# Optimization experiments

Measured on AMD Instinct MI355X. Metric: run time of the kernel, lower is better.

Reference implementation:

```python
import jax, jax.numpy as jnp
import numpy as np

HALF = 6.0
MAXC = 63.0
M_EMA = 0.999

def _pooled_ema(feature, pre, fea):
    # feature: [b,c,64,64]; pre: [b,21,2] float coords; fea: [21,c] EMA state
    b, c, H, W = feature.shape
    x = pre[..., 0]
    y = pre[..., 1]
    # torch: clamp then .int() (truncation == floor for non-negative values)
    down = jnp.maximum(y - HALF, 0.0).astype(jnp.int32)   # [b,21]
    left = jnp.maximum(x - HALF, 0.0).astype(jnp.int32)
    upper = jnp.minimum(y + HALF, MAXC).astype(jnp.int32)
    right = jnp.minimum(x + HALF, MAXC).astype(jnp.int32)
    # divisor uses inclusive window size (s1*s2), even though the torch slice
    # feature[:, left:right, down:upper] is exclusive at right/upper (faithful quirk)
    s = ((upper - down + 1) * (right - left + 1)).astype(feature.dtype)  # [b,21]
    # integral image (padded) -> rectangle sum over [left,right) x [down,upper)
    P = jnp.pad(jnp.cumsum(jnp.cumsum(feature, axis=2), axis=3),
                ((0, 0), (0, 0), (1, 0), (1, 0)))  # [b,c,H+1,W+1]
    bi = jnp.arange(b)[:, None]  # [b,1] broadcasts with [b,21] indices
    rect = (P[bi, :, right, upper] - P[bi, :, left, upper]
            - P[bi, :, right, down] + P[bi, :, left, down])  # [b,21,c]
    f4 = rect / s[..., None]          # per-landmark average pool [b,21,c]
    fea_c = f4.mean(axis=0)           # average over batch -> [21,c]
    return M_EMA * fea_c + (1.0 - M_EMA) * fea


def setup_inputs() -> dict:
    key = jax.random.key(0)
    k1, k2, k3, k4 = jax.random.split(key, 4)
    b, c, H, W, L = 64, 256, 64, 64, 21
    f1 = jax.random.uniform(k1, (b, c, H, W), dtype=jnp.float32)
    f2 = jax.random.uniform(k2, (b, c, H, W), dtype=jnp.float32)
    pre1 = jax.random.uniform(k3, (b, L, 2), dtype=jnp.float32) * 63.0
    pre2 = jax.random.uniform(k4, (b, L, 2), dtype=jnp.float32) * 63.0
    fea1 = jnp.zeros((L, c), dtype=jnp.float32)
    fea2 = jnp.zeros((L, c), dtype=jnp.float32)
    return {"f1": f1, "f2": f2, "pre1": pre1, "pre2": pre2,
            "fea1": fea1, "fea2": fea2}


def reference(f1, f2, pre1, pre2, fea1, fea2):
    fea_c1 = _pooled_ema(f1, pre1, fea1)               # [21,c]
    log_p = jax.nn.log_softmax(fea_c1, axis=-1)
    fea_c2 = _pooled_ema(f2, pre2, fea2)               # [21,c]
    q = fea_c2 / fea_c2.sum(axis=-1, keepdims=True)
    # KLDivLoss(reduction='none'): q * (log q - log_p), zero where q == 0
    kl = jnp.where(q > 0, q * (jnp.log(jnp.where(q > 0, q, 1.0)) - log_p), 0.0)
    return kl.sum(axis=-1).mean()
```

## Files before the change

kernel.cpp:

```cpp
#include <hip/hip_runtime.h>

#define NL 21
#define NC 256
#define NB 64
#define PSTRIDE 68
#define PPB 16

__global__ __launch_bounds__(256) void pool_kernel(
    const float* __restrict__ f1, const float* __restrict__ f2,
    const float* __restrict__ pre1, const float* __restrict__ pre2,
    float* __restrict__ part1, float* __restrict__ part2) {
    const int p0   = blockIdx.x * PPB;
    const int feat = p0 >> 14;
    const int b    = (p0 >> 8) & 63;
    const int c0   = p0 & 255;
    const float* __restrict__ base = (feat ? f2 : f1) + (size_t)(b * NC + c0) * 4096;
    const float* __restrict__ pre  = feat ? pre2 : pre1;
    float* __restrict__ outp       = (feat ? part2 : part1) + (size_t)b * NL * NC;

    __shared__ float buf[2][64 * PSTRIDE];
    __shared__ float fold[256];
    __shared__ int s_left[NL], s_right[NL], s_down[NL], s_upper[NL];
    __shared__ float s_invs[NL];

    const int t = threadIdx.x;

    if (t < NL) {
        const float x = pre[(b * NL + t) * 2 + 0];
        const float y = pre[(b * NL + t) * 2 + 1];
        const int down  = (int)fmaxf(y - 6.0f, 0.0f);
        const int left  = (int)fmaxf(x - 6.0f, 0.0f);
        const int upper = (int)fminf(y + 6.0f, 63.0f);
        const int right = (int)fminf(x + 6.0f, 63.0f);
        s_left[t] = left; s_right[t] = right; s_down[t] = down; s_upper[t] = upper;
        s_invs[t] = 1.0f / (float)((upper - down + 1) * (right - left + 1));
    }

    float4 v0, v1, v2, v3;
    {
        const float4* __restrict__ src = (const float4*)base;
        v0 = src[t]; v1 = src[t + 256]; v2 = src[t + 512]; v3 = src[t + 768];
    }
    {
        float* d = buf[0];
        *(float4*)&d[((t        ) >> 4) * PSTRIDE + ((t        ) & 15) * 4] = v0;
        *(float4*)&d[((t + 256) >> 4) * PSTRIDE + ((t + 256) & 15) * 4] = v1;
        *(float4*)&d[((t + 512) >> 4) * PSTRIDE + ((t + 512) & 15) * 4] = v2;
        *(float4*)&d[((t + 768) >> 4) * PSTRIDE + ((t + 768) & 15) * 4] = v3;
    }
    __syncthreads();

    for (int i = 0; i < PPB; ++i) {
        const int cur = i & 1;
        if (i + 1 < PPB) {
            const float4* __restrict__ src = (const float4*)(base + (size_t)(i + 1) * 4096);
            v0 = src[t]; v1 = src[t + 256]; v2 = src[t + 512]; v3 = src[t + 768];
        }
        float val = 0.0f;
        if (t < NL * 12) {
            const int l = t / 12;
            const int kk = t - l * 12;
            const int h = s_left[l] + kk;
            if (h < s_right[l]) {
                const float* row = &buf[cur][h * PSTRIDE];
                const int d = s_down[l], u = s_upper[l];
                float s = 0.0f;
                for (int w = d; w < u; ++w) s += row[w];
                val = s;
            }
        }
        fold[t] = val;
        __syncthreads();
        if (t < NL) {
            float r = 0.0f;
#pragma unroll
            for (int kk = 0; kk < 12; ++kk) r += fold[t * 12 + kk];
            outp[t * NC + (c0 + i)] = r * s_invs[t];
        }
        if (i + 1 < PPB) {
            float* d = buf[1 - cur];
            *(float4*)&d[((t        ) >> 4) * PSTRIDE + ((t        ) & 15) * 4] = v0;
            *(float4*)&d[((t + 256) >> 4) * PSTRIDE + ((t + 256) & 15) * 4] = v1;
            *(float4*)&d[((t + 512) >> 4) * PSTRIDE + ((t + 512) & 15) * 4] = v2;
            *(float4*)&d[((t + 768) >> 4) * PSTRIDE + ((t + 768) & 15) * 4] = v3;
        }
        __syncthreads();
    }
}

__global__ __launch_bounds__(256) void reduce_kernel(
    const float* __restrict__ part1, const float* __restrict__ part2,
    const float* __restrict__ fea1, const float* __restrict__ fea2,
    float* __restrict__ sc ) {
    const int f = blockIdx.x / NL;
    const int l = blockIdx.x - f * NL;
    const int c = threadIdx.x;
    const float* __restrict__ part = f ? part2 : part1;
    const float* __restrict__ fea  = f ? fea2 : fea1;
    float s = 0.0f;
    for (int b = 0; b < NB; ++b) s += part[((size_t)b * NL + l) * NC + c];
    sc[(f * NL + l) * NC + c] = 0.999f * (s * (1.0f / 64.0f)) + 0.001f * fea[l * NC + c];
}

__global__ __launch_bounds__(256) void finish_kernel(const float* __restrict__ sc,
                                                     float* __restrict__ out) {
    const int t = threadIdx.x;
    const int wave = t >> 6, lane = t & 63;
    __shared__ float rowkl[NL];

    for (int l = wave; l < NL; l += 4) {
        const float* __restrict__ r1 = &sc[l * NC];
        const float* __restrict__ r2 = &sc[(NL + l) * NC];
        float x1[4], x2[4];
#pragma unroll
        for (int j = 0; j < 4; ++j) { x1[j] = r1[lane + 64 * j]; x2[j] = r2[lane + 64 * j]; }

        float m  = fmaxf(fmaxf(x1[0], x1[1]), fmaxf(x1[2], x1[3]));
        float s2 = x2[0] + x2[1] + x2[2] + x2[3];
#pragma unroll
        for (int o = 32; o > 0; o >>= 1) {
            m  = fmaxf(m, __shfl_xor(m, o, 64));
            s2 += __shfl_xor(s2, o, 64);
        }
        float es = 0.0f;
#pragma unroll
        for (int j = 0; j < 4; ++j) es += __expf(x1[j] - m);
#pragma unroll
        for (int o = 32; o > 0; o >>= 1) es += __shfl_xor(es, o, 64);
        const float logZ = m + logf(es);
        const float inv_s2 = 1.0f / s2;

        float kl = 0.0f;
#pragma unroll
        for (int j = 0; j < 4; ++j) {
            const float q = x2[j] * inv_s2;
            if (q > 0.0f) kl += q * (logf(q) - (x1[j] - logZ));
        }
#pragma unroll
        for (int o = 32; o > 0; o >>= 1) kl += __shfl_xor(kl, o, 64);
        if (lane == 0) rowkl[l] = kl;
    }
    __syncthreads();
    if (t == 0) {
        float tot = 0.0f;
        for (int l = 0; l < NL; ++l) tot += rowkl[l];
        out[0] = tot / 21.0f;
    }
}

extern "C" void kernel_launch(void* const* d_in, const int* in_sizes, int n_in,
                              void* d_out, int out_size, void* d_ws, size_t ws_size,
                              hipStream_t stream) {
    const float* f1   = (const float*)d_in[0];
    const float* f2   = (const float*)d_in[1];
    const float* pre1 = (const float*)d_in[2];
    const float* pre2 = (const float*)d_in[3];
    const float* fea1 = (const float*)d_in[4];
    const float* fea2 = (const float*)d_in[5];
    float* out = (float*)d_out;

    float* part1 = (float*)d_ws;
    float* part2 = part1 + (size_t)NB * NL * NC;
    float* sc    = part2 + (size_t)NB * NL * NC;

    pool_kernel<<<dim3(2 * NB * NC / PPB), 256, 0, stream>>>(f1, f2, pre1, pre2, part1, part2);
    reduce_kernel<<<dim3(2 * NL), 256, 0, stream>>>(part1, part2, fea1, fea2, sc);
    finish_kernel<<<1, 256, 0, stream>>>(sc, out);
}
```

Before: 524.3 us.

## Reduce landmark windows per wave with shuffles and single LDS buffer

Each wave now handles a subset of landmarks, with lanes mapped to window columns and row groups, and reduces the window sum via wave shuffles instead of serial per-thread row loops plus a shared-memory fold. The double LDS buffer and fold array are dropped, padding stride changes, and an occupancy hint of 8 blocks is added. This aims to cut serial LDS loops and shared memory to raise occupancy, at the cost of more shuffle work per landmark and idle lanes for small windows.

```diff
diff --git a/kernel.cpp b/kernel.cpp
--- a/kernel.cpp
+++ b/kernel.cpp
@@ -3,10 +3,10 @@
 #define NL 21
 #define NC 256
 #define NB 64
-#define PSTRIDE 68
+#define PSTRIDE 72
 #define PPB 16
 
-__global__ __launch_bounds__(256) void pool_kernel(
+__global__ __launch_bounds__(256, 8) void pool_kernel(
     const float* __restrict__ f1, const float* __restrict__ f2,
     const float* __restrict__ pre1, const float* __restrict__ pre2,
     float* __restrict__ part1, float* __restrict__ part2) {
@@ -18,12 +18,15 @@
     const float* __restrict__ pre  = feat ? pre2 : pre1;
     float* __restrict__ outp       = (feat ? part2 : part1) + (size_t)b * NL * NC;
 
-    __shared__ float buf[2][64 * PSTRIDE];
-    __shared__ float fold[256];
+    __shared__ float buf[64 * PSTRIDE];
     __shared__ int s_left[NL], s_right[NL], s_down[NL], s_upper[NL];
     __shared__ float s_invs[NL];
 
-    const int t = threadIdx.x;
+    const int t    = threadIdx.x;
+    const int wv   = t >> 6;
+    const int lane = t & 63;
+    const int rr   = lane >> 4;
+    const int cc   = lane & 15;
 
     if (t < NL) {
         const float x = pre[(b * NL + t) * 2 + 0];
@@ -40,49 +43,41 @@
     {
         const float4* __restrict__ src = (const float4*)base;
         v0 = src[t]; v1 = src[t + 256]; v2 = src[t + 512]; v3 = src[t + 768];
-    }
-    {
-        float* d = buf[0];
-        *(float4*)&d[((t        ) >> 4) * PSTRIDE + ((t        ) & 15) * 4] = v0;
-        *(float4*)&d[((t + 256) >> 4) * PSTRIDE + ((t + 256) & 15) * 4] = v1;
-        *(float4*)&d[((t + 512) >> 4) * PSTRIDE + ((t + 512) & 15) * 4] = v2;
-        *(float4*)&d[((t + 768) >> 4) * PSTRIDE + ((t + 768) & 15) * 4] = v3;
+        *(float4*)&buf[((t      ) >> 4) * PSTRIDE + ((t      ) & 15) * 4] = v0;
+        *(float4*)&buf[((t + 256) >> 4) * PSTRIDE + ((t + 256) & 15) * 4] = v1;
+        *(float4*)&buf[((t + 512) >> 4) * PSTRIDE + ((t + 512) & 15) * 4] = v2;
+        *(float4*)&buf[((t + 768) >> 4) * PSTRIDE + ((t + 768) & 15) * 4] = v3;
     }
     __syncthreads();
 
     for (int i = 0; i < PPB; ++i) {
-        const int cur = i & 1;
         if (i + 1 < PPB) {
             const float4* __restrict__ src = (const float4*)(base + (size_t)(i + 1) * 4096);
             v0 = src[t]; v1 = src[t + 256]; v2 = src[t + 512]; v3 = src[t + 768];
         }
-        float val = 0.0f;
-        if (t < NL * 12) {
-            const int l = t / 12;
-            const int kk = t - l * 12;
-            const int h = s_left[l] + kk;
-            if (h < s_right[l]) {
-                const float* row = &buf[cur][h * PSTRIDE];
-                const int d = s_down[l], u = s_upper[l];
-                float s = 0.0f;
-                for (int w = d; w < u; ++w) s += row[w];
-                val = s;
+        for (int l = wv; l < NL; l += 4) {
+            const int d = s_down[l], u = s_upper[l];
+            const int L = s_left[l], R = s_right[l];
+            const int col = d + cc;
+            float s = 0.0f;
+            if (col < u) {
+                const float* __restrict__ rowp = &buf[col];
+#pragma unroll
+                for (int p = 0; p < 3; ++p) {
+                    const int row = L + p * 4 + rr;
+                    if (row < R) s += rowp[row * PSTRIDE];
+                }
             }
+#pragma unroll
+            for (int o = 32; o > 0; o >>= 1) s += __shfl_xor(s, o, 64);
+            if (lane == 0) outp[l * NC + (c0 + i)] = s * s_invs[l];
         }
-        fold[t] = val;
         __syncthreads();
-        if (t < NL) {
-            float r = 0.0f;
-#pragma unroll
-            for (int kk = 0; kk < 12; ++kk) r += fold[t * 12 + kk];
-            outp[t * NC + (c0 + i)] = r * s_invs[t];
-        }
         if (i + 1 < PPB) {
-            float* d = buf[1 - cur];
-            *(float4*)&d[((t        ) >> 4) * PSTRIDE + ((t        ) & 15) * 4] = v0;
-            *(float4*)&d[((t + 256) >> 4) * PSTRIDE + ((t + 256) & 15) * 4] = v1;
-            *(float4*)&d[((t + 512) >> 4) * PSTRIDE + ((t + 512) & 15) * 4] = v2;
-            *(float4*)&d[((t + 768) >> 4) * PSTRIDE + ((t + 768) & 15) * 4] = v3;
+            *(float4*)&buf[((t      ) >> 4) * PSTRIDE + ((t      ) & 15) * 4] = v0;
+            *(float4*)&buf[((t + 256) >> 4) * PSTRIDE + ((t + 256) & 15) * 4] = v1;
+            *(float4*)&buf[((t + 512) >> 4) * PSTRIDE + ((t + 512) & 15) * 4] = v2;
+            *(float4*)&buf[((t + 768) >> 4) * PSTRIDE + ((t + 768) & 15) * 4] = v3;
         }
         __syncthreads();
     }
```

Result: slower. 542.4 us (+3.5%).
